# Kernel optimization log

Measured on AMD Instinct MI355X. Metric: run time of the kernel, lower is better.

Reference implementation:

```python
import jax, jax.numpy as jnp
import numpy as np

N_NODES = 50000
N_EDGES = 800000
IN_FEATS = 1024
LAYERS = [128, 128]
EPS = 1e-5  # BatchNorm1d eps


def setup_inputs() -> dict:
    key = jax.random.key(0)
    ks = jax.random.split(key, 24)
    inp = {}
    inp["in_feat"] = jax.random.normal(ks[0], (N_NODES, IN_FEATS), jnp.float32)
    inp["src"] = jax.random.randint(ks[1], (N_EDGES,), 0, N_NODES, dtype=jnp.int32)
    inp["dst"] = jax.random.randint(ks[2], (N_EDGES,), 0, N_NODES, dtype=jnp.int32)
    dims = [IN_FEATS] + LAYERS
    i = 3
    for l in range(len(LAYERS)):
        din, dout = dims[l], dims[l + 1]
        s = 1.0 / np.sqrt(din)
        inp[f"W{l}"] = jax.random.uniform(ks[i], (din, dout), jnp.float32, -s, s); i += 1
        inp[f"b{l}"] = jnp.zeros((dout,), jnp.float32)
        inp[f"Wr{l}"] = jax.random.uniform(ks[i], (din, dout), jnp.float32, -s, s); i += 1
        inp[f"br{l}"] = jnp.zeros((dout,), jnp.float32)
        inp[f"gamma{l}"] = jnp.ones((dout,), jnp.float32)
        inp[f"beta{l}"] = jnp.zeros((dout,), jnp.float32)
        inp[f"mean{l}"] = jnp.zeros((dout,), jnp.float32)
        inp[f"var{l}"] = jnp.ones((dout,), jnp.float32)
    s = 1.0 / np.sqrt(LAYERS[-1])
    inp["Wd"] = jax.random.uniform(ks[i], (LAYERS[-1], 2), jnp.float32, -s, s)
    inp["bd"] = jnp.zeros((2,), jnp.float32)
    return inp


def gcn_layer(h, src, dst, W, b, Wr, br, gamma, beta, mean, var):
    # dgllife GCNLayer: GraphConv(norm='none', activation=relu) -> residual -> dropout(id, eval) -> BN(eval)
    msg = (h @ W)[src]                                        # [E, dout] gather of transformed src feats
    agg = jax.ops.segment_sum(msg, dst, num_segments=N_NODES)  # scatter-add to dst nodes
    new = jax.nn.relu(agg + b)                                 # GraphConv bias + activation
    res = jax.nn.relu(h @ Wr + br)                             # residual Linear + activation
    new = new + res
    return (new - mean) * jax.lax.rsqrt(var + EPS) * gamma + beta  # BatchNorm1d eval


def reference(in_feat, src, dst,
              W0, b0, Wr0, br0, gamma0, beta0, mean0, var0,
              W1, b1, Wr1, br1, gamma1, beta1, mean1, var1,
              Wd, bd):
    h = gcn_layer(in_feat, src, dst, W0, b0, Wr0, br0, gamma0, beta0, mean0, var0)
    h = gcn_layer(h, src, dst, W1, b1, Wr1, br1, gamma1, beta1, mean1, var1)
    logits = h @ Wd + bd                                       # [N, 2]
    return jax.nn.softmax(logits, axis=1)
```

## Files before the change

kernel.cpp:

```cpp
#include <hip/hip_runtime.h>
#include <math.h>

#define NNODES 50000
#define NEDGES 800000
#define KIN 1024
#define DH 128

typedef __bf16 bf16x8 __attribute__((ext_vector_type(8)));
typedef float floatx4 __attribute__((ext_vector_type(4)));

__global__ void k_zero2(int* __restrict__ a, int* __restrict__ b, int n) {
  int i = blockIdx.x * blockDim.x + threadIdx.x;
  if (i < n) { a[i] = 0; b[i] = 0; }
}

__global__ void k_hist(const int* __restrict__ dst, int* __restrict__ cnt, int E) {
  int i = blockIdx.x * blockDim.x + threadIdx.x;
  if (i < E) atomicAdd(&cnt[dst[i]], 1);
}

__global__ __launch_bounds__(1024) void k_scan_local(const int* __restrict__ cnt,
                                                     int* __restrict__ row_ptr,
                                                     int* __restrict__ bsum, int n) {
  __shared__ int sd[1024];
  int t = threadIdx.x;
  int i = blockIdx.x * 1024 + t;
  int v = (i < n) ? cnt[i] : 0;
  sd[t] = v;
  __syncthreads();
  for (int off = 1; off < 1024; off <<= 1) {
    int tv = (t >= off) ? sd[t - off] : 0;
    __syncthreads();
    sd[t] += tv;
    __syncthreads();
  }
  if (i < n) row_ptr[i] = sd[t] - v;
  if (t == 1023) bsum[blockIdx.x] = sd[t];
}

__global__ void k_scan_sums(const int* __restrict__ bsum, int* __restrict__ boff,
                            int nb, int* __restrict__ row_ptr, int n) {
  int lane = threadIdx.x;
  int v = (lane < nb) ? bsum[lane] : 0;
  int incl = v;
  for (int off = 1; off < 64; off <<= 1) {
    int t = __shfl_up(incl, off);
    if (lane >= off) incl += t;
  }
  boff[lane] = incl - v;
  if (lane == 63) row_ptr[n] = incl;
}

__global__ void k_scan_add(int* __restrict__ row_ptr, const int* __restrict__ boff, int n) {
  int i = blockIdx.x * blockDim.x + threadIdx.x;
  if (i < n) row_ptr[i] += boff[i >> 10];
}

__global__ void k_fill(const int* __restrict__ src, const int* __restrict__ dst,
                       const int* __restrict__ row_ptr, int* __restrict__ cursor,
                       int* __restrict__ csr_src, int E) {
  int i = blockIdx.x * blockDim.x + threadIdx.x;
  if (i < E) {
    int d = dst[i];
    int pos = row_ptr[d] + atomicAdd(&cursor[d], 1);
    csr_src[pos] = src[i];
  }
}

__global__ __launch_bounds__(256) void k_prepB(const float* __restrict__ W,
                                               const float* __restrict__ Wr,
                                               __bf16* __restrict__ Bt, int K, int kbits) {
  int id = blockIdx.x * 256 + threadIdx.x;
  int k = id & (K - 1);
  int n = id >> kbits;
  float v = (n < DH) ? W[(size_t)k * DH + n] : Wr[(size_t)k * DH + (n - DH)];
  Bt[(size_t)n * K + k] = (__bf16)v;
}

__device__ __forceinline__ void load_lds16(const void* g, void* l) {
  __builtin_amdgcn_global_load_lds(
      (const __attribute__((address_space(1))) unsigned int*)g,
      (__attribute__((address_space(3))) unsigned int*)l, 16, 0, 0);
}

template <typename AT, int K>
__global__ __launch_bounds__(512, 4) void k_gemm_mfma(
    const AT* __restrict__ X, const __bf16* __restrict__ Bt,
    const float* __restrict__ br, __bf16* __restrict__ XW,
    float* __restrict__ RES, int M) {
  __shared__ alignas(16) char smem[32768];
  const int tid = threadIdx.x;
  const int lane = tid & 63;
  const int w = tid >> 6;
  const int wr = w >> 2;
  const int wc = w & 3;
  const int l15 = lane & 15;
  const int quad = lane >> 4;
  const int bm0 = blockIdx.x * 64;
  constexpr int ROWB = (sizeof(AT) == 4) ? 256 : 128;
  constexpr int ABUF = 64 * ROWB;

  auto stageA = [&](int buf, int k0) {
    char* dst = smem + buf * ABUF;
    if constexpr (sizeof(AT) == 4) {
#pragma unroll
      for (int i = 0; i < 2; ++i) {
        const int r = w * 8 + i * 4 + (lane >> 4);
        int gr = bm0 + r; if (gr > M - 1) gr = M - 1;
        const int c = (lane & 15) ^ (r & 7);
        load_lds16((const char*)X + ((size_t)gr * K + k0 + c * 4) * 4,
                   dst + (w * 8 + i * 4) * 256);
      }
    } else {
      const int r = w * 8 + (lane >> 3);
      int gr = bm0 + r; if (gr > M - 1) gr = M - 1;
      const int c = (lane & 7) ^ (r & 7);
      load_lds16((const char*)X + ((size_t)gr * K + k0 + c * 8) * 2,
                 dst + w * 8 * 128);
    }
  };

  auto readA = [&](int buf, int mt, int ks) -> bf16x8 {
    const int r = wr * 32 + mt * 16 + l15;
    const char* rowp = smem + buf * ABUF + r * ROWB;
    if constexpr (sizeof(AT) == 4) {
      const int x = r & 7;
      const int c0 = ks * 8 + quad * 2;
      const floatx4 u = *(const floatx4*)(rowp + ((c0 ^ x) << 4));
      const floatx4 v = *(const floatx4*)(rowp + (((c0 + 1) ^ x) << 4));
      bf16x8 h;
      h[0] = (__bf16)u[0]; h[1] = (__bf16)u[1]; h[2] = (__bf16)u[2]; h[3] = (__bf16)u[3];
      h[4] = (__bf16)v[0]; h[5] = (__bf16)v[1]; h[6] = (__bf16)v[2]; h[7] = (__bf16)v[3];
      return h;
    } else {
      const int cc = ks * 4 + quad;
      return *(const bf16x8*)(rowp + ((cc ^ (r & 7)) << 4));
    }
  };

  floatx4 acc[2][4];
#pragma unroll
  for (int i = 0; i < 2; ++i)
#pragma unroll
    for (int j = 0; j < 4; ++j) acc[i][j] = (floatx4)0.f;

  stageA(0, 0);
  __syncthreads();

  constexpr int NS = K / 64;
  for (int s = 0; s < NS; ++s) {
    const int k0 = s * 64;
    const int buf = s & 1;
    if (s + 1 < NS) stageA(buf ^ 1, k0 + 64);
#pragma unroll
    for (int ks = 0; ks < 2; ++ks) {
      const bf16x8 a0 = readA(buf, 0, ks);
      const bf16x8 a1 = readA(buf, 1, ks);
#pragma unroll
      for (int nt = 0; nt < 4; ++nt) {
        const int n = wc * 64 + nt * 16 + l15;
        const bf16x8 bfrag =
            *(const bf16x8*)(Bt + (size_t)n * K + k0 + ks * 32 + quad * 8);
        acc[0][nt] = __builtin_amdgcn_mfma_f32_16x16x32_bf16(a0, bfrag, acc[0][nt], 0, 0, 0);
        acc[1][nt] = __builtin_amdgcn_mfma_f32_16x16x32_bf16(a1, bfrag, acc[1][nt], 0, 0, 0);
      }
    }
    __syncthreads();
  }

  float* Cb = (float*)smem;
#pragma unroll
  for (int half = 0; half < 2; ++half) {
    if (wr == half) {
#pragma unroll
      for (int mt = 0; mt < 2; ++mt)
#pragma unroll
        for (int nt = 0; nt < 4; ++nt)
#pragma unroll
          for (int r = 0; r < 4; ++r)
            Cb[(mt * 16 + quad * 4 + r) * 256 + wc * 64 + nt * 16 + l15] = acc[mt][nt][r];
    }
    __syncthreads();
    const int row = tid >> 4;
    const int seg = tid & 15;
    const int grow = bm0 + half * 32 + row;
    if (grow < M) {
      if (seg < 8) {
        const int c0 = seg * 16;
#pragma unroll
        for (int j = 0; j < 2; ++j) {
          const float4 v0 = *(const float4*)&Cb[row * 256 + c0 + j * 8];
          const float4 v1 = *(const float4*)&Cb[row * 256 + c0 + j * 8 + 4];
          bf16x8 h;
          h[0] = (__bf16)v0.x; h[1] = (__bf16)v0.y; h[2] = (__bf16)v0.z; h[3] = (__bf16)v0.w;
          h[4] = (__bf16)v1.x; h[5] = (__bf16)v1.y; h[6] = (__bf16)v1.z; h[7] = (__bf16)v1.w;
          *(bf16x8*)&XW[(size_t)grow * DH + c0 + j * 8] = h;
        }
      } else {
        const int c0 = (seg - 8) * 16;
#pragma unroll
        for (int j = 0; j < 4; ++j) {
          const float4 v = *(const float4*)&Cb[row * 256 + 128 + c0 + j * 4];
          const float4 bb = *(const float4*)&br[c0 + j * 4];
          *(float4*)&RES[(size_t)grow * DH + c0 + j * 4] =
              make_float4(fmaxf(v.x + bb.x, 0.f), fmaxf(v.y + bb.y, 0.f),
                          fmaxf(v.z + bb.z, 0.f), fmaxf(v.w + bb.w, 0.f));
        }
      }
    }
    __syncthreads();
  }
}

template <int MODE>
__global__ __launch_bounds__(256) void k_agg2(
    const __bf16* __restrict__ XW, const float* __restrict__ RES,
    const int* __restrict__ row_ptr, const int* __restrict__ csr_src,
    const float* __restrict__ b, const float* __restrict__ gamma,
    const float* __restrict__ beta, const float* __restrict__ mean,
    const float* __restrict__ var, const float* __restrict__ Wd,
    const float* __restrict__ bd, void* __restrict__ hout, int M) {
  const int node = (blockIdx.x << 2) + (threadIdx.x >> 6);
  const int lane = threadIdx.x & 63;
  if (node >= M) return;
  const int s = row_ptr[node], e = row_ptr[node + 1];
  const unsigned* xw = (const unsigned*)XW;
  float ax = 0.f, ay = 0.f;
  int i = s;
  for (; i + 3 < e; i += 4) {
    const int s0 = csr_src[i], s1 = csr_src[i + 1], s2 = csr_src[i + 2], s3 = csr_src[i + 3];
    const unsigned u0 = xw[(size_t)s0 * 64 + lane];
    const unsigned u1 = xw[(size_t)s1 * 64 + lane];
    const unsigned u2 = xw[(size_t)s2 * 64 + lane];
    const unsigned u3 = xw[(size_t)s3 * 64 + lane];
    ax += __uint_as_float(u0 << 16) + __uint_as_float(u1 << 16) +
          __uint_as_float(u2 << 16) + __uint_as_float(u3 << 16);
    ay += __uint_as_float(u0 & 0xffff0000u) + __uint_as_float(u1 & 0xffff0000u) +
          __uint_as_float(u2 & 0xffff0000u) + __uint_as_float(u3 & 0xffff0000u);
  }
  for (; i < e; ++i) {
    const unsigned u = xw[(size_t)csr_src[i] * 64 + lane];
    ax += __uint_as_float(u << 16);
    ay += __uint_as_float(u & 0xffff0000u);
  }
  const int f0 = lane << 1;
  const float2 bb = *(const float2*)&b[f0];
  const float2 rr = *(const float2*)&RES[(size_t)node * DH + f0];
  const float2 mm = *(const float2*)&mean[f0];
  const float2 vv = *(const float2*)&var[f0];
  const float2 gg = *(const float2*)&gamma[f0];
  const float2 be = *(const float2*)&beta[f0];
  const float x0 = fmaxf(ax + bb.x, 0.f) + rr.x;
  const float x1 = fmaxf(ay + bb.y, 0.f) + rr.y;
  const float y0 = (x0 - mm.x) * rsqrtf(vv.x + 1e-5f) * gg.x + be.x;
  const float y1 = (x1 - mm.y) * rsqrtf(vv.y + 1e-5f) * gg.y + be.y;
  if (MODE == 0) {
    union { __bf16 h[2]; unsigned u; } pk;
    pk.h[0] = (__bf16)y0;
    pk.h[1] = (__bf16)y1;
    ((unsigned*)hout)[(size_t)node * 64 + lane] = pk.u;
  } else {
    const float4 wv = *(const float4*)&Wd[f0 * 2];
    float l0 = y0 * wv.x + y1 * wv.z;
    float l1 = y0 * wv.y + y1 * wv.w;
#pragma unroll
    for (int off = 32; off > 0; off >>= 1) {
      l0 += __shfl_down(l0, off);
      l1 += __shfl_down(l1, off);
    }
    if (lane == 0) {
      l0 += bd[0];
      l1 += bd[1];
      const float m = fmaxf(l0, l1);
      const float e0 = expf(l0 - m), e1 = expf(l1 - m);
      const float inv = 1.f / (e0 + e1);
      float* out = (float*)hout;
      out[(size_t)node * 2] = e0 * inv;
      out[(size_t)node * 2 + 1] = e1 * inv;
    }
  }
}

extern "C" void kernel_launch(void* const* d_in, const int* in_sizes, int n_in,
                              void* d_out, int out_size, void* d_ws, size_t ws_size,
                              hipStream_t stream) {
  const float* in_feat = (const float*)d_in[0];
  const int* src = (const int*)d_in[1];
  const int* dst = (const int*)d_in[2];
  const float* W0 = (const float*)d_in[3];
  const float* b0 = (const float*)d_in[4];
  const float* Wr0 = (const float*)d_in[5];
  const float* br0 = (const float*)d_in[6];
  const float* gamma0 = (const float*)d_in[7];
  const float* beta0 = (const float*)d_in[8];
  const float* mean0 = (const float*)d_in[9];
  const float* var0 = (const float*)d_in[10];
  const float* W1 = (const float*)d_in[11];
  const float* b1 = (const float*)d_in[12];
  const float* Wr1 = (const float*)d_in[13];
  const float* br1 = (const float*)d_in[14];
  const float* gamma1 = (const float*)d_in[15];
  const float* beta1 = (const float*)d_in[16];
  const float* mean1 = (const float*)d_in[17];
  const float* var1 = (const float*)d_in[18];
  const float* Wd = (const float*)d_in[19];
  const float* bd = (const float*)d_in[20];
  float* out = (float*)d_out;

  char* ws = (char*)d_ws;
  size_t off = 0;
  auto alloc = [&](size_t bytes) {
    void* p = ws + off;
    off += (bytes + 255) & ~(size_t)255;
    return p;
  };
  __bf16* XWb = (__bf16*)alloc(sizeof(__bf16) * (size_t)NNODES * DH);
  __bf16* h1 = (__bf16*)alloc(sizeof(__bf16) * (size_t)NNODES * DH);
  float* RES = (float*)alloc(sizeof(float) * (size_t)NNODES * DH);
  int* cnt = (int*)alloc(sizeof(int) * NNODES);
  int* cursor = (int*)alloc(sizeof(int) * NNODES);
  int* row_ptr = (int*)alloc(sizeof(int) * (NNODES + 1));
  int* csr_src = (int*)alloc(sizeof(int) * NEDGES);
  int* bsum = (int*)alloc(sizeof(int) * 64);
  int* boff = (int*)alloc(sizeof(int) * 64);
  __bf16* Bt0 = (__bf16*)alloc(sizeof(__bf16) * 256 * KIN);
  __bf16* Bt1 = (__bf16*)alloc(sizeof(__bf16) * 256 * DH);

  const int nb = (NNODES + 1023) / 1024;
  k_zero2<<<(NNODES + 255) / 256, 256, 0, stream>>>(cnt, cursor, NNODES);
  k_hist<<<(NEDGES + 255) / 256, 256, 0, stream>>>(dst, cnt, NEDGES);
  k_scan_local<<<nb, 1024, 0, stream>>>(cnt, row_ptr, bsum, NNODES);
  k_scan_sums<<<1, 64, 0, stream>>>(bsum, boff, nb, row_ptr, NNODES);
  k_scan_add<<<(NNODES + 255) / 256, 256, 0, stream>>>(row_ptr, boff, NNODES);
  k_fill<<<(NEDGES + 255) / 256, 256, 0, stream>>>(src, dst, row_ptr, cursor, csr_src, NEDGES);

  k_prepB<<<KIN, 256, 0, stream>>>(W0, Wr0, Bt0, KIN, 10);
  k_prepB<<<DH, 256, 0, stream>>>(W1, Wr1, Bt1, DH, 7);

  const int ggrid = (NNODES + 63) / 64;
  const int agrid = (NNODES + 3) / 4;
  k_gemm_mfma<float, KIN><<<ggrid, 512, 0, stream>>>(in_feat, Bt0, br0, XWb, RES, NNODES);
  k_agg2<0><<<agrid, 256, 0, stream>>>(XWb, RES, row_ptr, csr_src, b0, gamma0, beta0,
                                       mean0, var0, nullptr, nullptr, h1, NNODES);
  k_gemm_mfma<__bf16, DH><<<ggrid, 512, 0, stream>>>(h1, Bt1, br1, XWb, RES, NNODES);
  k_agg2<1><<<agrid, 256, 0, stream>>>(XWb, RES, row_ptr, csr_src, b1, gamma1, beta1,
                                       mean1, var1, Wd, bd, out, NNODES);
}
```

Measured before the change: 618.7 us.

## Stage B tiles through LDS with a three-buffer async pipeline in MFMA GEMM

The GEMM kernel now loads B (weight) tiles into LDS with global_load_lds alongside the A tiles, instead of reading B fragments directly from global memory in the inner loop. It also moves from a double-buffered to a triple-buffered pipeline with explicit vmcnt waits and a single barrier per stage, prefetching two stages ahead. This is meant to hide global load latency and cut the redundant global B reads made by each wave. In exchange, LDS use per block grows to about 3x(32-48KB) and launch bounds drop to 2 blocks per CU, which lowers occupancy.

```diff
diff --git a/kernel.cpp b/kernel.cpp
--- a/kernel.cpp
+++ b/kernel.cpp
@@ -83,12 +83,18 @@
       (__attribute__((address_space(3))) unsigned int*)l, 16, 0, 0);
 }
 
+#define WAITV(N) asm volatile("s_waitcnt vmcnt(" #N ")" ::: "memory")
+
 template <typename AT, int K>
-__global__ __launch_bounds__(512, 4) void k_gemm_mfma(
+__global__ __launch_bounds__(512, 2) void k_gemm_mfma(
     const AT* __restrict__ X, const __bf16* __restrict__ Bt,
     const float* __restrict__ br, __bf16* __restrict__ XW,
     float* __restrict__ RES, int M) {
-  __shared__ alignas(16) char smem[32768];
+  constexpr int ROWB = (sizeof(AT) == 4) ? 256 : 128;
+  constexpr int ABUF = 64 * ROWB;
+  constexpr int BBUF = 256 * 64 * 2;
+  constexpr int TBUF = ABUF + BBUF;
+  __shared__ alignas(16) char smem[3 * TBUF];
   const int tid = threadIdx.x;
   const int lane = tid & 63;
   const int w = tid >> 6;
@@ -97,11 +103,8 @@
   const int l15 = lane & 15;
   const int quad = lane >> 4;
   const int bm0 = blockIdx.x * 64;
-  constexpr int ROWB = (sizeof(AT) == 4) ? 256 : 128;
-  constexpr int ABUF = 64 * ROWB;
-
-  auto stageA = [&](int buf, int k0) {
-    char* dst = smem + buf * ABUF;
+
+  auto stageA = [&](char* abase, int k0) {
     if constexpr (sizeof(AT) == 4) {
 #pragma unroll
       for (int i = 0; i < 2; ++i) {
@@ -109,20 +112,36 @@
         int gr = bm0 + r; if (gr > M - 1) gr = M - 1;
         const int c = (lane & 15) ^ (r & 7);
         load_lds16((const char*)X + ((size_t)gr * K + k0 + c * 4) * 4,
-                   dst + (w * 8 + i * 4) * 256);
+                   abase + (w * 8 + i * 4) * 256);
       }
     } else {
       const int r = w * 8 + (lane >> 3);
       int gr = bm0 + r; if (gr > M - 1) gr = M - 1;
       const int c = (lane & 7) ^ (r & 7);
       load_lds16((const char*)X + ((size_t)gr * K + k0 + c * 8) * 2,
-                 dst + w * 8 * 128);
-    }
-  };
-
-  auto readA = [&](int buf, int mt, int ks) -> bf16x8 {
+                 abase + w * 8 * 128);
+    }
+  };
+  auto stageB = [&](char* bbase, int k0) {
+#pragma unroll
+    for (int ii = 0; ii < 4; ++ii) {
+      const int wi = ii * 8 + w;
+      const int n = wi * 8 + (lane >> 3);
+      const int c = lane & 7;
+      const int cs = c ^ (n & 7);
+      load_lds16((const char*)Bt + (size_t)n * (K * 2) + (size_t)k0 * 2 + cs * 16,
+                 bbase + wi * 1024);
+    }
+  };
+  auto stage = [&](int s) {
+    char* base = smem + (s % 3) * TBUF;
+    stageA(base, s * 64);
+    stageB(base + ABUF, s * 64);
+  };
+
+  auto readA = [&](const char* abase, int mt, int ks) -> bf16x8 {
     const int r = wr * 32 + mt * 16 + l15;
-    const char* rowp = smem + buf * ABUF + r * ROWB;
+    const char* rowp = abase + r * ROWB;
     if constexpr (sizeof(AT) == 4) {
       const int x = r & 7;
       const int c0 = ks * 8 + quad * 2;
@@ -137,6 +156,11 @@
       return *(const bf16x8*)(rowp + ((cc ^ (r & 7)) << 4));
     }
   };
+  auto readB = [&](const char* bbase, int nt, int ks) -> bf16x8 {
+    const int n = wc * 64 + nt * 16 + l15;
+    const int ch = (ks * 4 + quad) ^ (n & 7);
+    return *(const bf16x8*)(bbase + n * 128 + ch * 16);
+  };
 
   floatx4 acc[2][4];
 #pragma unroll
@@ -144,29 +168,42 @@
 #pragma unroll
     for (int j = 0; j < 4; ++j) acc[i][j] = (floatx4)0.f;
 
-  stageA(0, 0);
+  constexpr int NS = K / 64;
+  stage(0);
+  stage(1);
+
+  for (int s = 0; s < NS; ++s) {
+    if (s == NS - 1) {
+      WAITV(0);
+    } else if constexpr (sizeof(AT) == 4) {
+      WAITV(6);
+    } else {
+      WAITV(5);
+    }
+    __builtin_amdgcn_s_barrier();
+    __builtin_amdgcn_sched_barrier(0);
+    if (s + 2 < NS) stage(s + 2);
+    const char* abase = smem + (s % 3) * TBUF;
+    const char* bbase = abase + ABUF;
+    bf16x8 af[2][2], bfr[4][2];
+#pragma unroll
+    for (int mt = 0; mt < 2; ++mt)
+#pragma unroll
+      for (int ks = 0; ks < 2; ++ks) af[mt][ks] = readA(abase, mt, ks);
+#pragma unroll
+    for (int nt = 0; nt < 4; ++nt)
+#pragma unroll
+      for (int ks = 0; ks < 2; ++ks) bfr[nt][ks] = readB(bbase, nt, ks);
+#pragma unroll
+    for (int ks = 0; ks < 2; ++ks)
+#pragma unroll
+      for (int mt = 0; mt < 2; ++mt)
+#pragma unroll
+        for (int nt = 0; nt < 4; ++nt)
+          acc[mt][nt] = __builtin_amdgcn_mfma_f32_16x16x32_bf16(af[mt][ks], bfr[nt][ks],
+                                                                acc[mt][nt], 0, 0, 0);
+  }
   __syncthreads();
-
-  constexpr int NS = K / 64;
-  for (int s = 0; s < NS; ++s) {
-    const int k0 = s * 64;
-    const int buf = s & 1;
-    if (s + 1 < NS) stageA(buf ^ 1, k0 + 64);
-#pragma unroll
-    for (int ks = 0; ks < 2; ++ks) {
-      const bf16x8 a0 = readA(buf, 0, ks);
-      const bf16x8 a1 = readA(buf, 1, ks);
-#pragma unroll
-      for (int nt = 0; nt < 4; ++nt) {
-        const int n = wc * 64 + nt * 16 + l15;
-        const bf16x8 bfrag =
-            *(const bf16x8*)(Bt + (size_t)n * K + k0 + ks * 32 + quad * 8);
-        acc[0][nt] = __builtin_amdgcn_mfma_f32_16x16x32_bf16(a0, bfrag, acc[0][nt], 0, 0, 0);
-        acc[1][nt] = __builtin_amdgcn_mfma_f32_16x16x32_bf16(a1, bfrag, acc[1][nt], 0, 0, 0);
-      }
-    }
-    __syncthreads();
-  }
 
   float* Cb = (float*)smem;
 #pragma unroll
```

New measurement: 551.5 us. 10.9% less time.
